# Optimization experiments

Hardware: AMD Instinct MI355X
Metric: run time of the kernel (lower is better)

Reference implementation:

```python
import jax, jax.numpy as jnp
import numpy as np

BATCH, N_IN, N_MID, N_OUT = 1048576, 64, 32, 10


def setup_inputs() -> dict:
    key = jax.random.key(0)
    k_x, k_w1, k_b1, k_w2, k_b2 = jax.random.split(key, 5)
    # scalar synapse weights k collectively form dense matrices; init like
    # Synapse.init_weight: uniform(-sqrt(1/fan_in), sqrt(1/fan_in))
    v1 = np.sqrt(1.0 / N_IN)
    v2 = np.sqrt(1.0 / N_MID)
    return {
        "x": jax.random.normal(k_x, (BATCH, N_IN), dtype=jnp.float32),
        "W1": jax.random.uniform(k_w1, (N_IN, N_MID), dtype=jnp.float32, minval=-v1, maxval=v1),
        "b1": jnp.zeros((N_MID,), dtype=jnp.float32),  # obtain_float_parameter inits to 0.0
        "W2": jax.random.uniform(k_w2, (N_MID, N_OUT), dtype=jnp.float32, minval=-v2, maxval=v2),
        "b2": jnp.zeros((N_OUT,), dtype=jnp.float32),
    }


def reference(x, W1, b1, W2, b2):
    # RegularNeuron: output = ReLU(b + sum_j k_j * input_j)  -> relu(x @ W1 + b1)
    h = jax.nn.relu(x @ W1 + b1)  # [batch, n_middle]
    # DestinationNeuron (no activation): y = b + sum_j k_j * h_j -> h @ W2 + b2
    y = h @ W2 + b2  # [batch, n_outputs]
    return y
```

## Files before the change

kernel.cpp:

```cpp
#include <hip/hip_runtime.h>


#define N_IN  64
#define N_MID 32
#define N_OUT 10

#define WAVES_PER_BLOCK 4
#define TILES_PER_WAVE  4
#define ROWS_PER_TILE   16
#define ROWS_PER_BLOCK  (WAVES_PER_BLOCK * TILES_PER_WAVE * ROWS_PER_TILE)
#define H_STRIDE        80

typedef short bf16x8 __attribute__((ext_vector_type(8)));
typedef float f32x4  __attribute__((ext_vector_type(4)));

static __device__ __forceinline__ short f2bf(float f) {
    __bf16 h = (__bf16)f;
    return __builtin_bit_cast(short, h);
}

__global__ __launch_bounds__(256)
void livenet_mfma(const float* __restrict__ x,
                  const float* __restrict__ W1,
                  const float* __restrict__ b1,
                  const float* __restrict__ W2,
                  const float* __restrict__ b2,
                  float* __restrict__ out,
                  int batch) {
    __shared__ unsigned char h_lds_all[WAVES_PER_BLOCK][ROWS_PER_TILE * H_STRIDE];

    const int lane = threadIdx.x & 63;
    const int wave = threadIdx.x >> 6;
    const int g    = lane >> 4;
    const int c    = lane & 15;

    unsigned char* h_lds = h_lds_all[wave];

    bf16x8 w1f[2][2];
    #pragma unroll
    for (int n = 0; n < 2; ++n)
        #pragma unroll
        for (int p = 0; p < 2; ++p)
            #pragma unroll
            for (int i = 0; i < 8; ++i) {
                int k = p * 32 + 8 * g + i;
                w1f[n][p][i] = f2bf(W1[k * N_MID + n * 16 + c]);
            }

    bf16x8 w2f;
    #pragma unroll
    for (int i = 0; i < 8; ++i) {
        int k = 8 * g + i;
        w2f[i] = (c < N_OUT) ? f2bf(W2[k * N_OUT + c]) : (short)0;
    }

    const float b1v0 = b1[c];
    const float b1v1 = b1[16 + c];
    const float b2v  = (c < N_OUT) ? b2[c] : 0.0f;

    const size_t wave_row0 = (size_t)blockIdx.x * ROWS_PER_BLOCK
                           + (size_t)wave * (TILES_PER_WAVE * ROWS_PER_TILE);

    for (int t = 0; t < TILES_PER_WAVE; ++t) {
        const size_t rb = wave_row0 + (size_t)t * ROWS_PER_TILE;
        if (rb + ROWS_PER_TILE > (size_t)batch) break;

        const float* xp = x + (rb + (size_t)c) * N_IN + 8 * g;
        const float4 v0 = *(const float4*)(xp + 0);
        const float4 v1 = *(const float4*)(xp + 4);
        const float4 v2 = *(const float4*)(xp + 32);
        const float4 v3 = *(const float4*)(xp + 36);

        bf16x8 a0, a1;
        a0[0] = f2bf(v0.x); a0[1] = f2bf(v0.y); a0[2] = f2bf(v0.z); a0[3] = f2bf(v0.w);
        a0[4] = f2bf(v1.x); a0[5] = f2bf(v1.y); a0[6] = f2bf(v1.z); a0[7] = f2bf(v1.w);
        a1[0] = f2bf(v2.x); a1[1] = f2bf(v2.y); a1[2] = f2bf(v2.z); a1[3] = f2bf(v2.w);
        a1[4] = f2bf(v3.x); a1[5] = f2bf(v3.y); a1[6] = f2bf(v3.z); a1[7] = f2bf(v3.w);

        f32x4 acc0 = {b1v0, b1v0, b1v0, b1v0};
        f32x4 acc1 = {b1v1, b1v1, b1v1, b1v1};
        acc0 = __builtin_amdgcn_mfma_f32_16x16x32_bf16(a0, w1f[0][0], acc0, 0, 0, 0);
        acc0 = __builtin_amdgcn_mfma_f32_16x16x32_bf16(a1, w1f[0][1], acc0, 0, 0, 0);
        acc1 = __builtin_amdgcn_mfma_f32_16x16x32_bf16(a0, w1f[1][0], acc1, 0, 0, 0);
        acc1 = __builtin_amdgcn_mfma_f32_16x16x32_bf16(a1, w1f[1][1], acc1, 0, 0, 0);

        #pragma unroll
        for (int r = 0; r < 4; ++r) {
            const int rowr = 4 * g + r;
            *(short*)(h_lds + rowr * H_STRIDE +      2 * c) = f2bf(fmaxf(acc0[r], 0.0f));
            *(short*)(h_lds + rowr * H_STRIDE + 32 + 2 * c) = f2bf(fmaxf(acc1[r], 0.0f));
        }
        __asm__ volatile("" ::: "memory");

        const bf16x8 hfrag = *(const bf16x8*)(h_lds + c * H_STRIDE + 16 * g);
        f32x4 acc2 = {b2v, b2v, b2v, b2v};
        acc2 = __builtin_amdgcn_mfma_f32_16x16x32_bf16(hfrag, w2f, acc2, 0, 0, 0);

        __asm__ volatile("" ::: "memory");

        if (c < N_OUT) {
            #pragma unroll
            for (int r = 0; r < 4; ++r) {
                out[(rb + 4 * g + r) * N_OUT + c] = acc2[r];
            }
        }
    }
}

extern "C" void kernel_launch(void* const* d_in, const int* in_sizes, int n_in,
                              void* d_out, int out_size, void* d_ws, size_t ws_size,
                              hipStream_t stream) {
    const float* x  = (const float*)d_in[0];
    const float* W1 = (const float*)d_in[1];
    const float* b1 = (const float*)d_in[2];
    const float* W2 = (const float*)d_in[3];
    const float* b2 = (const float*)d_in[4];
    float* out = (float*)d_out;

    int batch = in_sizes[0] / N_IN;
    int grid  = (batch + ROWS_PER_BLOCK - 1) / ROWS_PER_BLOCK;
    livenet_mfma<<<grid, 256, 0, stream>>>(x, W1, b1, W2, b2, out, batch);
}
```

Baseline: 63.67 us.

## Software-prefetch next x tile and pack hidden activations into 32-bit LDS stores

Adds a fast path for waves whose four tiles are all in bounds. In that path the loop is fully unrolled and the next tile's x float4 loads are issued before the current tile is computed, so global-load latency overlaps the MFMA work. Hidden activations are now stored as packed bf16 pairs in one 32-bit LDS write per row, which interleaves the two halves of the hidden layer. W2 fragment rows are permuted to match that interleaved order. This costs more registers for the prefetched values and duplicates the loop body in a tail path.

```diff
diff --git a/kernel.cpp b/kernel.cpp
--- a/kernel.cpp
+++ b/kernel.cpp
@@ -17,6 +17,12 @@
 static __device__ __forceinline__ short f2bf(float f) {
     __bf16 h = (__bf16)f;
     return __builtin_bit_cast(short, h);
+}
+
+static __device__ __forceinline__ unsigned pk2bf(float lo, float hi) {
+    unsigned l = (unsigned short)__builtin_bit_cast(unsigned short, (__bf16)lo);
+    unsigned h = (unsigned short)__builtin_bit_cast(unsigned short, (__bf16)hi);
+    return (h << 16) | l;
 }
 
 __global__ __launch_bounds__(256)
@@ -50,8 +56,9 @@
     bf16x8 w2f;
     #pragma unroll
     for (int i = 0; i < 8; ++i) {
-        int k = 8 * g + i;
-        w2f[i] = (c < N_OUT) ? f2bf(W2[k * N_OUT + c]) : (short)0;
+        int kpos = 8 * g + i;
+        int col  = (kpos & 1) * 16 + (kpos >> 1);
+        w2f[i] = (c < N_OUT) ? f2bf(W2[col * N_OUT + c]) : (short)0;
     }
 
     const float b1v0 = b1[c];
@@ -60,48 +67,109 @@
 
     const size_t wave_row0 = (size_t)blockIdx.x * ROWS_PER_BLOCK
                            + (size_t)wave * (TILES_PER_WAVE * ROWS_PER_TILE);
+    const bool full = (wave_row0 + TILES_PER_WAVE * ROWS_PER_TILE) <= (size_t)batch;
 
-    for (int t = 0; t < TILES_PER_WAVE; ++t) {
-        const size_t rb = wave_row0 + (size_t)t * ROWS_PER_TILE;
-        if (rb + ROWS_PER_TILE > (size_t)batch) break;
+    const float* xbase = x + (wave_row0 + (size_t)c) * N_IN + 8 * g;
 
-        const float* xp = x + (rb + (size_t)c) * N_IN + 8 * g;
-        const float4 v0 = *(const float4*)(xp + 0);
-        const float4 v1 = *(const float4*)(xp + 4);
-        const float4 v2 = *(const float4*)(xp + 32);
-        const float4 v3 = *(const float4*)(xp + 36);
-
-        bf16x8 a0, a1;
-        a0[0] = f2bf(v0.x); a0[1] = f2bf(v0.y); a0[2] = f2bf(v0.z); a0[3] = f2bf(v0.w);
-        a0[4] = f2bf(v1.x); a0[5] = f2bf(v1.y); a0[6] = f2bf(v1.z); a0[7] = f2bf(v1.w);
-        a1[0] = f2bf(v2.x); a1[1] = f2bf(v2.y); a1[2] = f2bf(v2.z); a1[3] = f2bf(v2.w);
-        a1[4] = f2bf(v3.x); a1[5] = f2bf(v3.y); a1[6] = f2bf(v3.z); a1[7] = f2bf(v3.w);
-
-        f32x4 acc0 = {b1v0, b1v0, b1v0, b1v0};
-        f32x4 acc1 = {b1v1, b1v1, b1v1, b1v1};
-        acc0 = __builtin_amdgcn_mfma_f32_16x16x32_bf16(a0, w1f[0][0], acc0, 0, 0, 0);
-        acc0 = __builtin_amdgcn_mfma_f32_16x16x32_bf16(a1, w1f[0][1], acc0, 0, 0, 0);
-        acc1 = __builtin_amdgcn_mfma_f32_16x16x32_bf16(a0, w1f[1][0], acc1, 0, 0, 0);
-        acc1 = __builtin_amdgcn_mfma_f32_16x16x32_bf16(a1, w1f[1][1], acc1, 0, 0, 0);
+    if (full) {
+        float4 v0 = *(const float4*)(xbase + 0);
+        float4 v1 = *(const float4*)(xbase + 4);
+        float4 v2 = *(const float4*)(xbase + 32);
+        float4 v3 = *(const float4*)(xbase + 36);
 
         #pragma unroll
-        for (int r = 0; r < 4; ++r) {
-            const int rowr = 4 * g + r;
-            *(short*)(h_lds + rowr * H_STRIDE +      2 * c) = f2bf(fmaxf(acc0[r], 0.0f));
-            *(short*)(h_lds + rowr * H_STRIDE + 32 + 2 * c) = f2bf(fmaxf(acc1[r], 0.0f));
-        }
-        __asm__ volatile("" ::: "memory");
+        for (int t = 0; t < TILES_PER_WAVE; ++t) {
+            float4 n0 = v0, n1 = v1, n2 = v2, n3 = v3;
+            if (t + 1 < TILES_PER_WAVE) {
+                const float* xp = xbase + (size_t)(t + 1) * ROWS_PER_TILE * N_IN;
+                n0 = *(const float4*)(xp + 0);
+                n1 = *(const float4*)(xp + 4);
+                n2 = *(const float4*)(xp + 32);
+                n3 = *(const float4*)(xp + 36);
+            }
 
-        const bf16x8 hfrag = *(const bf16x8*)(h_lds + c * H_STRIDE + 16 * g);
-        f32x4 acc2 = {b2v, b2v, b2v, b2v};
-        acc2 = __builtin_amdgcn_mfma_f32_16x16x32_bf16(hfrag, w2f, acc2, 0, 0, 0);
+            bf16x8 a0, a1;
+            a0[0] = f2bf(v0.x); a0[1] = f2bf(v0.y); a0[2] = f2bf(v0.z); a0[3] = f2bf(v0.w);
+            a0[4] = f2bf(v1.x); a0[5] = f2bf(v1.y); a0[6] = f2bf(v1.z); a0[7] = f2bf(v1.w);
+            a1[0] = f2bf(v2.x); a1[1] = f2bf(v2.y); a1[2] = f2bf(v2.z); a1[3] = f2bf(v2.w);
+            a1[4] = f2bf(v3.x); a1[5] = f2bf(v3.y); a1[6] = f2bf(v3.z); a1[7] = f2bf(v3.w);
 
-        __asm__ volatile("" ::: "memory");
+            f32x4 acc0 = {b1v0, b1v0, b1v0, b1v0};
+            f32x4 acc1 = {b1v1, b1v1, b1v1, b1v1};
+            acc0 = __builtin_amdgcn_mfma_f32_16x16x32_bf16(a0, w1f[0][0], acc0, 0, 0, 0);
+            acc0 = __builtin_amdgcn_mfma_f32_16x16x32_bf16(a1, w1f[0][1], acc0, 0, 0, 0);
+            acc1 = __builtin_amdgcn_mfma_f32_16x16x32_bf16(a0, w1f[1][0], acc1, 0, 0, 0);
+            acc1 = __builtin_amdgcn_mfma_f32_16x16x32_bf16(a1, w1f[1][1], acc1, 0, 0, 0);
 
-        if (c < N_OUT) {
             #pragma unroll
             for (int r = 0; r < 4; ++r) {
-                out[(rb + 4 * g + r) * N_OUT + c] = acc2[r];
+                const int rowr = 4 * g + r;
+                *(unsigned*)(h_lds + rowr * H_STRIDE + 4 * c) =
+                    pk2bf(fmaxf(acc0[r], 0.0f), fmaxf(acc1[r], 0.0f));
+            }
+            __asm__ volatile("" ::: "memory");
+
+            const bf16x8 hfrag = *(const bf16x8*)(h_lds + c * H_STRIDE + 16 * g);
+            f32x4 acc2 = {b2v, b2v, b2v, b2v};
+            acc2 = __builtin_amdgcn_mfma_f32_16x16x32_bf16(hfrag, w2f, acc2, 0, 0, 0);
+
+            __asm__ volatile("" ::: "memory");
+
+            if (c < N_OUT) {
+                const size_t rb = wave_row0 + (size_t)t * ROWS_PER_TILE;
+                float* op = out + (rb + 4 * g) * N_OUT + c;
+                op[0 * N_OUT] = acc2[0];
+                op[1 * N_OUT] = acc2[1];
+                op[2 * N_OUT] = acc2[2];
+                op[3 * N_OUT] = acc2[3];
+            }
+
+            v0 = n0; v1 = n1; v2 = n2; v3 = n3;
+        }
+    } else {
+        for (int t = 0; t < TILES_PER_WAVE; ++t) {
+            const size_t rb = wave_row0 + (size_t)t * ROWS_PER_TILE;
+            if (rb + ROWS_PER_TILE > (size_t)batch) break;
+
+            const float* xp = xbase + (size_t)t * ROWS_PER_TILE * N_IN;
+            float4 v0 = *(const float4*)(xp + 0);
+            float4 v1 = *(const float4*)(xp + 4);
+            float4 v2 = *(const float4*)(xp + 32);
+            float4 v3 = *(const float4*)(xp + 36);
+
+            bf16x8 a0, a1;
+            a0[0] = f2bf(v0.x); a0[1] = f2bf(v0.y); a0[2] = f2bf(v0.z); a0[3] = f2bf(v0.w);
+            a0[4] = f2bf(v1.x); a0[5] = f2bf(v1.y); a0[6] = f2bf(v1.z); a0[7] = f2bf(v1.w);
+            a1[0] = f2bf(v2.x); a1[1] = f2bf(v2.y); a1[2] = f2bf(v2.z); a1[3] = f2bf(v2.w);
+            a1[4] = f2bf(v3.x); a1[5] = f2bf(v3.y); a1[6] = f2bf(v3.z); a1[7] = f2bf(v3.w);
+
+            f32x4 acc0 = {b1v0, b1v0, b1v0, b1v0};
+            f32x4 acc1 = {b1v1, b1v1, b1v1, b1v1};
+            acc0 = __builtin_amdgcn_mfma_f32_16x16x32_bf16(a0, w1f[0][0], acc0, 0, 0, 0);
+            acc0 = __builtin_amdgcn_mfma_f32_16x16x32_bf16(a1, w1f[0][1], acc0, 0, 0, 0);
+            acc1 = __builtin_amdgcn_mfma_f32_16x16x32_bf16(a0, w1f[1][0], acc1, 0, 0, 0);
+            acc1 = __builtin_amdgcn_mfma_f32_16x16x32_bf16(a1, w1f[1][1], acc1, 0, 0, 0);
+
+            #pragma unroll
+            for (int r = 0; r < 4; ++r) {
+                const int rowr = 4 * g + r;
+                *(unsigned*)(h_lds + rowr * H_STRIDE + 4 * c) =
+                    pk2bf(fmaxf(acc0[r], 0.0f), fmaxf(acc1[r], 0.0f));
+            }
+            __asm__ volatile("" ::: "memory");
+
+            const bf16x8 hfrag = *(const bf16x8*)(h_lds + c * H_STRIDE + 16 * g);
+            f32x4 acc2 = {b2v, b2v, b2v, b2v};
+            acc2 = __builtin_amdgcn_mfma_f32_16x16x32_bf16(hfrag, w2f, acc2, 0, 0, 0);
+
+            __asm__ volatile("" ::: "memory");
+
+            if (c < N_OUT) {
+                float* op = out + (rb + 4 * g) * N_OUT + c;
+                op[0 * N_OUT] = acc2[0];
+                op[1 * N_OUT] = acc2[1];
+                op[2 * N_OUT] = acc2[2];
+                op[3 * N_OUT] = acc2[3];
             }
         }
     }
```

New measurement: 66.58 us. 1.05x slower.
